# Kernel optimization log

Hardware: AMD Instinct MI355X
Metric: run time of the kernel (lower is better)

## Reference

```python
import jax, jax.numpy as jnp
import numpy as np

TOP_K = 512  # int(node_num * K) = int(2048 * 0.25)
NEG = -1.0e12
SLOPE = 0.01  # nn.LeakyReLU default negative_slope


def setup_inputs() -> dict:
    key = jax.random.key(0)
    k1, k2, k3, k4 = jax.random.split(key, 4)
    B, N, in_c, out_c, gs = 8, 2048, 128, 128, 128
    x = jax.random.normal(k1, (B, N, in_c), dtype=jnp.float32)
    W = jax.random.normal(k2, (in_c, out_c), dtype=jnp.float32) * (1.0 / np.sqrt(in_c))
    a = jax.random.normal(k3, (2 * out_c, 1), dtype=jnp.float32) * (1.0 / np.sqrt(2 * out_c))
    GL = jax.random.normal(k4, (N, gs), dtype=jnp.float32) * (1.0 / np.sqrt(gs))
    return {"x": x, "W": W, "a": a, "GL": GL}


def reference(x, W, a, GL):
    B, N, _ = x.shape
    out_c = W.shape[1]
    # learned adjacency: softmax(relu(GL GL^T)) + I  -> [N, N]
    adj = jax.nn.softmax(jax.nn.relu(GL @ GL.T), axis=-1) + jnp.eye(N, dtype=GL.dtype)
    h = x @ W  # [B, N, out_c]
    # e[b,i,j] = LeakyReLU( [h_i ; h_j] . a ) = LeakyReLU( h_i.a1 + h_j.a2 )
    # (avoids materializing the [B, N*N, 2*out_c] concat of the original)
    a1, a2 = a[:out_c, 0], a[out_c:, 0]
    e = jax.nn.leaky_relu((h @ a1)[:, :, None] + (h @ a2)[:, None, :], SLOPE)  # [B,N,N]
    att = jnp.where(adj[None] > 0, e, NEG)
    # top-k along dim=1 (rows, per column j): transpose so that axis is last
    att_t = jnp.swapaxes(att, 1, 2)  # [B, Nj, Ni]
    _, idx = jax.lax.top_k(att_t, TOP_K)  # idx: [B, Nj, TOP_K]
    b_ix = jnp.arange(B)[:, None, None]
    j_ix = jnp.arange(N)[None, :, None]
    mask_t = jnp.zeros_like(att_t).at[b_ix, j_ix, idx].set(1.0)
    mask = jnp.swapaxes(mask_t, 1, 2)  # [B, Ni, Nj]
    att = jax.nn.softmax(att * mask, axis=2)
    h_prime = jax.nn.relu(att @ h)  # [B, N, out_c]
    return jnp.swapaxes(h_prime, -2, -1)  # [B, out_c, N]
```

## Files before the change

### kernel.cpp

```cpp
#include <hip/hip_runtime.h>
#include <math.h>


#define B_ 8
#define N_ 2048
#define C_ 128
#define TOPK_ 512
#define NCH_ 32
#define CL_ 64
#define NP1_ 2052
#define SORTB_ (2 * B_)

#define H_OFF    ((size_t)0)
#define P_OFF    (H_OFF + (size_t)B_*N_*C_)
#define Q_OFF    (P_OFF + (size_t)B_*N_)
#define QS_OFF   (Q_OFF + (size_t)B_*N_)
#define US_OFF   (QS_OFF + (size_t)B_*N_)
#define VS_OFF   (US_OFF + (size_t)B_*N_)
#define SRT_OFF  (VS_OFF + (size_t)B_*N_)
#define SUS_OFF  (SRT_OFF + (size_t)B_*N_)
#define PVS_OFF  (SUS_OFF + (size_t)B_*NP1_)
#define SUL_OFF  (PVS_OFF + (size_t)B_*NP1_)
#define PVL_OFF  (SUL_OFF + (size_t)B_*N_*128)
#define TOTU_OFF (PVL_OFF + (size_t)B_*N_*128)
#define TOTV_OFF (TOTU_OFF + (size_t)B_*NCH_*128)
#define MPART_OFF (TOTV_OFF + (size_t)B_*NCH_*128)
#define PTHR_OFF (MPART_OFF + (size_t)B_*32*C_)
#define ITHR_OFF (PTHR_OFF + (size_t)B_)

__device__ __forceinline__ unsigned enc_f(float f) {
  unsigned b = __float_as_uint(f);
  return b ^ ((b >> 31) ? 0xFFFFFFFFu : 0x80000000u);
}
__device__ __forceinline__ float dec_f(unsigned e) {
  unsigned b = (e & 0x80000000u) ? (e ^ 0x80000000u) : ~e;
  return __uint_as_float(b);
}
__device__ __forceinline__ unsigned long long sxor64(unsigned long long v, int m) {
  int lo = __shfl_xor((int)(unsigned)(v & 0xffffffffULL), m, 64);
  int hi = __shfl_xor((int)(unsigned)(v >> 32), m, 64);
  return (((unsigned long long)(unsigned)hi) << 32) | (unsigned)lo;
}
__device__ __forceinline__ void cswap2(unsigned long long& a, unsigned long long& b, bool up) {
  bool sw = up ? (a > b) : (b > a);
  if (sw) { unsigned long long tm = a; a = b; b = tm; }
}

__global__ __launch_bounds__(256) void k_pq(const float* __restrict__ x,
                                            const float* __restrict__ W,
                                            const float* __restrict__ a,
                                            float* __restrict__ p,
                                            float* __restrict__ q) {
  __shared__ float al[256];
  __shared__ float wa1[128], wa2[128];
  const int t = threadIdx.x;
  const int r0 = blockIdx.x * 64;
  al[t] = a[t];
  __syncthreads();
  if (t < 128) {
    const float* Wr = W + (size_t)t * 128;
    float s1 = 0.f, s2 = 0.f;
#pragma unroll
    for (int j = 0; j < 128; j += 4) {
      float4 wv = *(const float4*)(Wr + j);
      s1 = fmaf(wv.x, al[j + 0], s1);
      s1 = fmaf(wv.y, al[j + 1], s1);
      s1 = fmaf(wv.z, al[j + 2], s1);
      s1 = fmaf(wv.w, al[j + 3], s1);
      s2 = fmaf(wv.x, al[128 + j + 0], s2);
      s2 = fmaf(wv.y, al[128 + j + 1], s2);
      s2 = fmaf(wv.z, al[128 + j + 2], s2);
      s2 = fmaf(wv.w, al[128 + j + 3], s2);
    }
    wa1[t] = s1; wa2[t] = s2;
  }
  __syncthreads();
  const int row = t >> 2, part = t & 3;
  const float* xr = x + (size_t)(r0 + row) * 128 + part * 32;
  const float* w1 = wa1 + part * 32;
  const float* w2 = wa2 + part * 32;
  float sp = 0.f, sq = 0.f;
#pragma unroll
  for (int i = 0; i < 8; ++i) {
    float4 xv = *(const float4*)(xr + 4 * i);
    float4 w1v = *(const float4*)(w1 + 4 * i);
    float4 w2v = *(const float4*)(w2 + 4 * i);
    sp = fmaf(xv.x, w1v.x, sp); sp = fmaf(xv.y, w1v.y, sp);
    sp = fmaf(xv.z, w1v.z, sp); sp = fmaf(xv.w, w1v.w, sp);
    sq = fmaf(xv.x, w2v.x, sq); sq = fmaf(xv.y, w2v.y, sq);
    sq = fmaf(xv.z, w2v.z, sq); sq = fmaf(xv.w, w2v.w, sq);
  }
  sp += __shfl_xor(sp, 1, 64); sp += __shfl_xor(sp, 2, 64);
  sq += __shfl_xor(sq, 1, 64); sq += __shfl_xor(sq, 2, 64);
  if (part == 0) { p[r0 + row] = sp; q[r0 + row] = sq; }
}

__global__ __launch_bounds__(512, 4) void k_fuse(
    const float* __restrict__ x, const float* __restrict__ W,
    float* __restrict__ h, float* __restrict__ mpart,
    const float* __restrict__ q, const float* __restrict__ p,
    float* __restrict__ q_s, float* __restrict__ u_s, float* __restrict__ v_s,
    int* __restrict__ srt, float* __restrict__ SUS, float* __restrict__ PVS,
    float* __restrict__ pthr, int* __restrict__ ithr) {
  union __align__(16) SMem {
    struct { float Wl[64 * 128]; float xl[64 * 68]; } g;
    struct { unsigned long long sh[N_]; float2 sa[512]; float2 sb[512]; } s;
  };
  __shared__ SMem sm;
  const int blk = blockIdx.x, t = threadIdx.x;

  if (blk < SORTB_) {
    const bool isP = blk >= B_;
    const int b = isP ? blk - B_ : blk;
    const float* src = isP ? p : q;
    float4 f4 = *(const float4*)(src + b * N_ + 4 * t);
    unsigned k0 = enc_f(f4.x), k1 = enc_f(f4.y), k2 = enc_f(f4.z), k3 = enc_f(f4.w);
    if (isP) { k0 = ~k0; k1 = ~k1; k2 = ~k2; k3 = ~k3; }
    unsigned long long r[4];
    r[0] = ((unsigned long long)k0 << 32) | (unsigned)(4 * t);
    r[1] = ((unsigned long long)k1 << 32) | (unsigned)(4 * t + 1);
    r[2] = ((unsigned long long)k2 << 32) | (unsigned)(4 * t + 2);
    r[3] = ((unsigned long long)k3 << 32) | (unsigned)(4 * t + 3);

    cswap2(r[0], r[1], true);
    cswap2(r[2], r[3], false);
    {
      const bool up4 = (t & 1) == 0;
      cswap2(r[0], r[2], up4); cswap2(r[1], r[3], up4);
      cswap2(r[0], r[1], up4); cswap2(r[2], r[3], up4);
    }
    for (int k = 8; k <= N_; k <<= 1) {
      const bool up = ((4 * t) & k) == 0;
      int j = k >> 1;
      for (; j >= 256; j >>= 1) {
        *(ulonglong2*)(sm.s.sh + 4 * t) = make_ulonglong2(r[0], r[1]);
        *(ulonglong2*)(sm.s.sh + 4 * t + 2) = make_ulonglong2(r[2], r[3]);
        __syncthreads();
        int pt = t ^ (j >> 2);
        ulonglong2 pa = *(const ulonglong2*)(sm.s.sh + 4 * pt);
        ulonglong2 pb = *(const ulonglong2*)(sm.s.sh + 4 * pt + 2);
        bool lower = (t & (j >> 2)) == 0;
        bool kmin = (up == lower);
        r[0] = kmin ? (r[0] < pa.x ? r[0] : pa.x) : (r[0] > pa.x ? r[0] : pa.x);
        r[1] = kmin ? (r[1] < pa.y ? r[1] : pa.y) : (r[1] > pa.y ? r[1] : pa.y);
        r[2] = kmin ? (r[2] < pb.x ? r[2] : pb.x) : (r[2] > pb.x ? r[2] : pb.x);
        r[3] = kmin ? (r[3] < pb.y ? r[3] : pb.y) : (r[3] > pb.y ? r[3] : pb.y);
        __syncthreads();
      }
      for (; j >= 4; j >>= 1) {
        int ld = j >> 2;
        unsigned long long p0 = sxor64(r[0], ld), p1 = sxor64(r[1], ld);
        unsigned long long p2 = sxor64(r[2], ld), p3 = sxor64(r[3], ld);
        bool lower = (t & ld) == 0;
        bool kmin = (up == lower);
        r[0] = kmin ? (r[0] < p0 ? r[0] : p0) : (r[0] > p0 ? r[0] : p0);
        r[1] = kmin ? (r[1] < p1 ? r[1] : p1) : (r[1] > p1 ? r[1] : p1);
        r[2] = kmin ? (r[2] < p2 ? r[2] : p2) : (r[2] > p2 ? r[2] : p2);
        r[3] = kmin ? (r[3] < p3 ? r[3] : p3) : (r[3] > p3 ? r[3] : p3);
      }
      cswap2(r[0], r[2], up); cswap2(r[1], r[3], up);
      cswap2(r[0], r[1], up); cswap2(r[2], r[3], up);
    }

    if (isP) {
      if (t == 127) {
        unsigned key = (unsigned)(r[3] >> 32);
        pthr[b] = dec_f(~key);
        ithr[b] = (int)(unsigned)(r[3] & 0xffffffffULL);
      }
      return;
    }
    float v[4], u[4], w[4]; int id[4];
#pragma unroll
    for (int s = 0; s < 4; ++s) {
      v[s] = dec_f((unsigned)(r[s] >> 32));
      id[s] = (int)(unsigned)(r[s] & 0xffffffffULL);
      u[s] = __expf(v[s]);
      w[s] = __expf(0.01f * v[s]);
    }
    *(float4*)(q_s + b * N_ + 4 * t) = make_float4(v[0], v[1], v[2], v[3]);
    *(float4*)(u_s + b * N_ + 4 * t) = make_float4(u[0], u[1], u[2], u[3]);
    *(float4*)(v_s + b * N_ + 4 * t) = make_float4(w[0], w[1], w[2], w[3]);
    *(int4*)(srt + b * N_ + 4 * t) = make_int4(id[0], id[1], id[2], id[3]);
    float pu = u[0] + u[1] + u[2] + u[3];
    float pw = w[0] + w[1] + w[2] + w[3];
    sm.s.sa[511 - t].x = pu;
    sm.s.sa[t].y = pw;
    __syncthreads();
    float2* cur = sm.s.sa; float2* nxt = sm.s.sb;
    for (int off = 1; off < 512; off <<= 1) {
      float2 vv = cur[t];
      if (t >= off) { float2 o = cur[t - off]; vv.x += o.x; vv.y += o.y; }
      nxt[t] = vv;
      __syncthreads();
      float2* tmp = cur; cur = nxt; nxt = tmp;
    }
    float PSt = cur[511 - t].x;
    float PPt = cur[t].y;
    float su0 = PSt;
    float su1 = su0 - u[0];
    float su2 = su1 - u[1];
    float su3 = su2 - u[2];
    *(float4*)(SUS + (size_t)b * NP1_ + 4 * t) = make_float4(su0, su1, su2, su3);
    float pv3 = PPt - w[3];
    float pv2 = pv3 - w[2];
    float pv1 = pv2 - w[1];
    float pv0 = pv1 - w[0];
    *(float4*)(PVS + (size_t)b * NP1_ + 4 * t) = make_float4(pv0, pv1, pv2, pv3);
    if (t == 511) {
      SUS[(size_t)b * NP1_ + N_] = 0.f;
      PVS[(size_t)b * NP1_ + N_] = PPt;
    }
    return;
  }

  float* Wl = sm.g.Wl;
  float* xl = sm.g.xl;
  const int g = blk - SORTB_;
  const int r0 = g * 64;
  const int cg = t & 15, rp = (t >> 4) & 15;
  const bool act = t < 256;
  float acc[4][8];
#pragma unroll
  for (int r = 0; r < 4; ++r)
#pragma unroll
    for (int j = 0; j < 8; ++j) acc[r][j] = 0.f;

  for (int kc = 0; kc < 2; ++kc) {
    __syncthreads();
    const float4* W4 = (const float4*)(W + (size_t)kc * 64 * 128);
    float4* Wl4 = (float4*)Wl;
#pragma unroll
    for (int i = 0; i < 4; ++i) Wl4[t + 512 * i] = W4[t + 512 * i];
#pragma unroll
    for (int i = 0; i < 2; ++i) {
      int idx = t + 512 * i;
      int row = idx >> 4, c4i = idx & 15;
      float4 v = *(const float4*)(x + (size_t)(r0 + row) * 128 + kc * 64 + c4i * 4);
      ((float4*)xl)[row * 17 + c4i] = v;
    }
    __syncthreads();
    if (act) {
      for (int k = 0; k < 64; ++k) {
        const float4* Wr = (const float4*)(Wl + k * 128);
        float4 w0 = Wr[cg];
        float4 w1 = Wr[cg + 16];
#pragma unroll
        for (int r = 0; r < 4; ++r) {
          float xv = xl[(4 * rp + r) * 68 + k];
          acc[r][0] = fmaf(xv, w0.x, acc[r][0]);
          acc[r][1] = fmaf(xv, w0.y, acc[r][1]);
          acc[r][2] = fmaf(xv, w0.z, acc[r][2]);
          acc[r][3] = fmaf(xv, w0.w, acc[r][3]);
          acc[r][4] = fmaf(xv, w1.x, acc[r][4]);
          acc[r][5] = fmaf(xv, w1.y, acc[r][5]);
          acc[r][6] = fmaf(xv, w1.z, acc[r][6]);
          acc[r][7] = fmaf(xv, w1.w, acc[r][7]);
        }
      }
    }
  }
  const int c0 = 4 * cg, c1 = 4 * cg + 64;
  size_t hb = (size_t)r0 * 128;
  __syncthreads();
  float* scratch = xl;
  if (act) {
#pragma unroll
    for (int r = 0; r < 4; ++r) {
      int row = 4 * rp + r;
      *(float4*)(h + hb + (size_t)row * 128 + c0) =
          make_float4(acc[r][0], acc[r][1], acc[r][2], acc[r][3]);
      *(float4*)(h + hb + (size_t)row * 128 + c1) =
          make_float4(acc[r][4], acc[r][5], acc[r][6], acc[r][7]);
    }
#pragma unroll
    for (int j = 0; j < 4; ++j) {
      scratch[rp * 128 + c0 + j] = acc[0][j] + acc[1][j] + acc[2][j] + acc[3][j];
      scratch[rp * 128 + c1 + j] = acc[0][4 + j] + acc[1][4 + j] + acc[2][4 + j] + acc[3][4 + j];
    }
  }
  __syncthreads();
  if (t < 128) {
    float s = 0.f;
#pragma unroll
    for (int rr = 0; rr < 16; ++rr) s += scratch[rr * 128 + t];
    mpart[(size_t)g * 128 + t] = s;
  }
}

__global__ __launch_bounds__(256) void k_scanA(const float* __restrict__ h,
                                               const float* __restrict__ u_s,
                                               const float* __restrict__ v_s,
                                               const int* __restrict__ srt,
                                               float* __restrict__ SUl,
                                               float* __restrict__ PVl,
                                               float* __restrict__ totU,
                                               float* __restrict__ totV) {
  __shared__ float hl[CL_][128];
  __shared__ float ul[CL_], vl[CL_];
  __shared__ int sl[CL_];
  const int b = blockIdx.x >> 5, ch = blockIdx.x & 31;
  const int t = threadIdx.x;
  const int base = b * N_ + ch * CL_;
  if (t < CL_) { ul[t] = u_s[base + t]; vl[t] = v_s[base + t]; sl[t] = srt[base + t]; }
  __syncthreads();
  {
    const int c4 = t & 31, rr = t >> 5;
#pragma unroll
    for (int i = 0; i < 8; ++i) {
      int tt = rr + 8 * i;
      float4 v = *(const float4*)(h + ((size_t)b * N_ + sl[tt]) * 128 + 4 * c4);
      *(float4*)(&hl[tt][4 * c4]) = v;
    }
  }
  __syncthreads();
  if (t < 128) {
    const int c = t;
    float run = 0.f;
    for (int tt = CL_ - 1; tt >= 0; --tt) {
      run = fmaf(ul[tt], hl[tt][c], run);
      SUl[((size_t)(base + tt)) * 128 + c] = run;
    }
    totU[(size_t)(b * NCH_ + ch) * 128 + c] = run;
  } else {
    const int c = t - 128;
    float run2 = 0.f;
    for (int tt = 0; tt < CL_; ++tt) {
      PVl[((size_t)(base + tt)) * 128 + c] = run2;
      run2 = fmaf(vl[tt], hl[tt][c], run2);
    }
    totV[(size_t)(b * NCH_ + ch) * 128 + c] = run2;
  }
}

__global__ __launch_bounds__(256) void k_out(const float* __restrict__ p,
                                             const float* __restrict__ q_s,
                                             const float* __restrict__ pthr,
                                             const int* __restrict__ ithr,
                                             const float* __restrict__ SUS,
                                             const float* __restrict__ PVS,
                                             const float* __restrict__ SUl,
                                             const float* __restrict__ PVl,
                                             const float* __restrict__ totU,
                                             const float* __restrict__ totV,
                                             const float* __restrict__ mpart,
                                             float* __restrict__ out) {
  __shared__ float qs_l[N_];
  __shared__ float res[64 * 129];
  __shared__ float CSUs[(NCH_ + 1) * 128];
  __shared__ float CPVs[(NCH_ + 1) * 128];
  __shared__ float mr[128];
  __shared__ float A_s[64], B_s[64], invD[64];
  __shared__ int lo_s[64], keep_s[64];
  const int b = blockIdx.x >> 5, tile = blockIdx.x & 31;
  const int t = threadIdx.x;
  const int i0 = tile * 64;
  for (int i = t; i < N_; i += 256) qs_l[i] = q_s[b * N_ + i];
  if (t < 128) {
    float ms = 0.f;
#pragma unroll
    for (int j = 0; j < 32; ++j) ms += mpart[(size_t)(b * 32 + j) * 128 + t];
    mr[t] = fmaxf(ms * (1.0f / (float)N_), 0.f);
    float s = 0.f;
    CSUs[NCH_ * 128 + t] = 0.f;
    for (int cc = NCH_ - 1; cc >= 0; --cc) {
      s += totU[(size_t)(b * NCH_ + cc) * 128 + t];
      CSUs[cc * 128 + t] = s;
    }
  } else {
    const int c2 = t - 128;
    float s2 = 0.f;
    for (int cc = 0; cc < NCH_; ++cc) {
      CPVs[cc * 128 + c2] = s2;
      s2 += totV[(size_t)(b * NCH_ + cc) * 128 + c2];
    }
    CPVs[NCH_ * 128 + c2] = s2;
  }
  __syncthreads();
  if (t < 64) {
    float pv = p[b * N_ + i0 + t];
    float thrv = pthr[b]; int thri = ithr[b];
    bool keep = (pv > thrv) || (pv == thrv && (i0 + t) <= thri);
    keep_s[t] = keep ? 1 : 0;
    float thr = -pv;
    int lo = 0, hi = N_;
    while (lo < hi) { int mid = (lo + hi) >> 1; if (qs_l[mid] < thr) lo = mid + 1; else hi = mid; }
    lo_s[t] = lo;
    float A = __expf(pv), Bv = __expf(0.01f * pv);
    A_s[t] = A; B_s[t] = Bv;
    float sus = SUS[(size_t)b * NP1_ + lo];
    float pvs = PVS[(size_t)b * NP1_ + lo];
    invD[t] = 1.0f / fmaf(A, sus, Bv * pvs);
  }
  __syncthreads();
  const int half = t >> 7, c = t & 127;
#pragma unroll 4
  for (int ii2 = 0; ii2 < 64; ii2 += 2) {
    int ii = ii2 + half;
    float outv;
    if (keep_s[ii]) {
      int lo = lo_s[ii];
      float A = A_s[ii], Bv = B_s[ii];
      float suc, pvc;
      if (lo < N_) {
        int chn = lo >> 6;
        size_t ro = ((size_t)(b * N_ + lo)) * 128;
        suc = SUl[ro + c] + CSUs[(chn + 1) * 128 + c];
        pvc = PVl[ro + c] + CPVs[chn * 128 + c];
      } else {
        suc = 0.f;
        pvc = CPVs[NCH_ * 128 + c];
      }
      outv = fmaxf(fmaf(A, suc, Bv * pvc) * invD[ii], 0.f);
    } else {
      outv = mr[c];
    }
    res[ii * 129 + c] = outv;
  }
  __syncthreads();
#pragma unroll
  for (int pass = 0; pass < 8; ++pass) {
    int cc = (t >> 4) + pass * 16;
    int ii4 = (t & 15) * 4;
    float4 v;
    v.x = res[(ii4 + 0) * 129 + cc];
    v.y = res[(ii4 + 1) * 129 + cc];
    v.z = res[(ii4 + 2) * 129 + cc];
    v.w = res[(ii4 + 3) * 129 + cc];
    *(float4*)(out + ((size_t)(b * C_ + cc)) * N_ + i0 + ii4) = v;
  }
}

extern "C" void kernel_launch(void* const* d_in, const int* in_sizes, int n_in,
                              void* d_out, int out_size, void* d_ws, size_t ws_size,
                              hipStream_t stream) {
  (void)in_sizes; (void)n_in; (void)out_size; (void)ws_size;
  const float* x = (const float*)d_in[0];
  const float* W = (const float*)d_in[1];
  const float* a = (const float*)d_in[2];
  float* out = (float*)d_out;
  float* ws = (float*)d_ws;

  float* h    = ws + H_OFF;
  float* p    = ws + P_OFF;
  float* q    = ws + Q_OFF;
  float* q_s  = ws + QS_OFF;
  float* u_s  = ws + US_OFF;
  float* v_s  = ws + VS_OFF;
  int*   srt  = (int*)(ws + SRT_OFF);
  float* SUS  = ws + SUS_OFF;
  float* PVS  = ws + PVS_OFF;
  float* SUl  = ws + SUL_OFF;
  float* PVl  = ws + PVL_OFF;
  float* totU = ws + TOTU_OFF;
  float* totV = ws + TOTV_OFF;
  float* mpart = ws + MPART_OFF;
  float* pthr = ws + PTHR_OFF;
  int*   ithr = (int*)(ws + ITHR_OFF);

  k_pq<<<dim3((B_ * N_) / 64), dim3(256), 0, stream>>>(x, W, a, p, q);
  k_fuse<<<dim3(SORTB_ + (B_ * N_) / 64), dim3(512), 0, stream>>>(
      x, W, h, mpart, q, p, q_s, u_s, v_s, srt, SUS, PVS, pthr, ithr);
  k_scanA<<<dim3(B_ * NCH_), dim3(256), 0, stream>>>(h, u_s, v_s, srt, SUl, PVl, totU, totV);
  k_out<<<dim3(B_ * 32), dim3(256), 0, stream>>>(p, q_s, pthr, ithr, SUS, PVS, SUl, PVl, totU, totV, mpart, out);
}
```

Measured before the change: 106.3 us.

## Replace per-batch bitonic sorts with parallel rank-counting across 256 blocks

Drops the 16 single-block bitonic sorts of q and p, which ran with many block-wide barriers. In their place, 256 blocks compute each element's rank, its lower-bound position and its top-k membership by brute-force counting over the row in shared memory, then scatter into sorted order. The prefix sums of the exponentials move into extra blocks of the scan kernel, and the binary search in k_out becomes a load of a packed word. This trades O(N^2) comparisons for much more parallelism and fewer serialized sync steps on the critical path.

```diff
diff --git a/kernel.cpp b/kernel.cpp
--- a/kernel.cpp
+++ b/kernel.cpp
@@ -9,13 +9,13 @@
 #define NCH_ 32
 #define CL_ 64
 #define NP1_ 2052
-#define SORTB_ (2 * B_)
+#define RANKB_ 256
 
 #define H_OFF    ((size_t)0)
 #define P_OFF    (H_OFF + (size_t)B_*N_*C_)
 #define Q_OFF    (P_OFF + (size_t)B_*N_)
-#define QS_OFF   (Q_OFF + (size_t)B_*N_)
-#define US_OFF   (QS_OFF + (size_t)B_*N_)
+#define LOK_OFF  (Q_OFF + (size_t)B_*N_)
+#define US_OFF   (LOK_OFF + (size_t)B_*N_)
 #define VS_OFF   (US_OFF + (size_t)B_*N_)
 #define SRT_OFF  (VS_OFF + (size_t)B_*N_)
 #define SUS_OFF  (SRT_OFF + (size_t)B_*N_)
@@ -25,26 +25,6 @@
 #define TOTU_OFF (PVL_OFF + (size_t)B_*N_*128)
 #define TOTV_OFF (TOTU_OFF + (size_t)B_*NCH_*128)
 #define MPART_OFF (TOTV_OFF + (size_t)B_*NCH_*128)
-#define PTHR_OFF (MPART_OFF + (size_t)B_*32*C_)
-#define ITHR_OFF (PTHR_OFF + (size_t)B_)
-
-__device__ __forceinline__ unsigned enc_f(float f) {
-  unsigned b = __float_as_uint(f);
-  return b ^ ((b >> 31) ? 0xFFFFFFFFu : 0x80000000u);
-}
-__device__ __forceinline__ float dec_f(unsigned e) {
-  unsigned b = (e & 0x80000000u) ? (e ^ 0x80000000u) : ~e;
-  return __uint_as_float(b);
-}
-__device__ __forceinline__ unsigned long long sxor64(unsigned long long v, int m) {
-  int lo = __shfl_xor((int)(unsigned)(v & 0xffffffffULL), m, 64);
-  int hi = __shfl_xor((int)(unsigned)(v >> 32), m, 64);
-  return (((unsigned long long)(unsigned)hi) << 32) | (unsigned)lo;
-}
-__device__ __forceinline__ void cswap2(unsigned long long& a, unsigned long long& b, bool up) {
-  bool sw = up ? (a > b) : (b > a);
-  if (sw) { unsigned long long tm = a; a = b; b = tm; }
-}
 
 __global__ __launch_bounds__(256) void k_pq(const float* __restrict__ x,
                                             const float* __restrict__ W,
@@ -99,124 +79,58 @@
     const float* __restrict__ x, const float* __restrict__ W,
     float* __restrict__ h, float* __restrict__ mpart,
     const float* __restrict__ q, const float* __restrict__ p,
-    float* __restrict__ q_s, float* __restrict__ u_s, float* __restrict__ v_s,
-    int* __restrict__ srt, float* __restrict__ SUS, float* __restrict__ PVS,
-    float* __restrict__ pthr, int* __restrict__ ithr) {
+    float* __restrict__ u_s, float* __restrict__ v_s,
+    int* __restrict__ srt, int* __restrict__ lok) {
   union __align__(16) SMem {
     struct { float Wl[64 * 128]; float xl[64 * 68]; } g;
-    struct { unsigned long long sh[N_]; float2 sa[512]; float2 sb[512]; } s;
+    struct { float ql[N_]; float pl[N_]; } r;
   };
   __shared__ SMem sm;
   const int blk = blockIdx.x, t = threadIdx.x;
 
-  if (blk < SORTB_) {
-    const bool isP = blk >= B_;
-    const int b = isP ? blk - B_ : blk;
-    const float* src = isP ? p : q;
-    float4 f4 = *(const float4*)(src + b * N_ + 4 * t);
-    unsigned k0 = enc_f(f4.x), k1 = enc_f(f4.y), k2 = enc_f(f4.z), k3 = enc_f(f4.w);
-    if (isP) { k0 = ~k0; k1 = ~k1; k2 = ~k2; k3 = ~k3; }
-    unsigned long long r[4];
-    r[0] = ((unsigned long long)k0 << 32) | (unsigned)(4 * t);
-    r[1] = ((unsigned long long)k1 << 32) | (unsigned)(4 * t + 1);
-    r[2] = ((unsigned long long)k2 << 32) | (unsigned)(4 * t + 2);
-    r[3] = ((unsigned long long)k3 << 32) | (unsigned)(4 * t + 3);
-
-    cswap2(r[0], r[1], true);
-    cswap2(r[2], r[3], false);
-    {
-      const bool up4 = (t & 1) == 0;
-      cswap2(r[0], r[2], up4); cswap2(r[1], r[3], up4);
-      cswap2(r[0], r[1], up4); cswap2(r[2], r[3], up4);
-    }
-    for (int k = 8; k <= N_; k <<= 1) {
-      const bool up = ((4 * t) & k) == 0;
-      int j = k >> 1;
-      for (; j >= 256; j >>= 1) {
-        *(ulonglong2*)(sm.s.sh + 4 * t) = make_ulonglong2(r[0], r[1]);
-        *(ulonglong2*)(sm.s.sh + 4 * t + 2) = make_ulonglong2(r[2], r[3]);
-        __syncthreads();
-        int pt = t ^ (j >> 2);
-        ulonglong2 pa = *(const ulonglong2*)(sm.s.sh + 4 * pt);
-        ulonglong2 pb = *(const ulonglong2*)(sm.s.sh + 4 * pt + 2);
-        bool lower = (t & (j >> 2)) == 0;
-        bool kmin = (up == lower);
-        r[0] = kmin ? (r[0] < pa.x ? r[0] : pa.x) : (r[0] > pa.x ? r[0] : pa.x);
-        r[1] = kmin ? (r[1] < pa.y ? r[1] : pa.y) : (r[1] > pa.y ? r[1] : pa.y);
-        r[2] = kmin ? (r[2] < pb.x ? r[2] : pb.x) : (r[2] > pb.x ? r[2] : pb.x);
-        r[3] = kmin ? (r[3] < pb.y ? r[3] : pb.y) : (r[3] > pb.y ? r[3] : pb.y);
-        __syncthreads();
-      }
-      for (; j >= 4; j >>= 1) {
-        int ld = j >> 2;
-        unsigned long long p0 = sxor64(r[0], ld), p1 = sxor64(r[1], ld);
-        unsigned long long p2 = sxor64(r[2], ld), p3 = sxor64(r[3], ld);
-        bool lower = (t & ld) == 0;
-        bool kmin = (up == lower);
-        r[0] = kmin ? (r[0] < p0 ? r[0] : p0) : (r[0] > p0 ? r[0] : p0);
-        r[1] = kmin ? (r[1] < p1 ? r[1] : p1) : (r[1] > p1 ? r[1] : p1);
-        r[2] = kmin ? (r[2] < p2 ? r[2] : p2) : (r[2] > p2 ? r[2] : p2);
-        r[3] = kmin ? (r[3] < p3 ? r[3] : p3) : (r[3] > p3 ? r[3] : p3);
-      }
-      cswap2(r[0], r[2], up); cswap2(r[1], r[3], up);
-      cswap2(r[0], r[1], up); cswap2(r[2], r[3], up);
-    }
-
-    if (isP) {
-      if (t == 127) {
-        unsigned key = (unsigned)(r[3] >> 32);
-        pthr[b] = dec_f(~key);
-        ithr[b] = (int)(unsigned)(r[3] & 0xffffffffULL);
-      }
-      return;
-    }
-    float v[4], u[4], w[4]; int id[4];
-#pragma unroll
-    for (int s = 0; s < 4; ++s) {
-      v[s] = dec_f((unsigned)(r[s] >> 32));
-      id[s] = (int)(unsigned)(r[s] & 0xffffffffULL);
-      u[s] = __expf(v[s]);
-      w[s] = __expf(0.01f * v[s]);
-    }
-    *(float4*)(q_s + b * N_ + 4 * t) = make_float4(v[0], v[1], v[2], v[3]);
-    *(float4*)(u_s + b * N_ + 4 * t) = make_float4(u[0], u[1], u[2], u[3]);
-    *(float4*)(v_s + b * N_ + 4 * t) = make_float4(w[0], w[1], w[2], w[3]);
-    *(int4*)(srt + b * N_ + 4 * t) = make_int4(id[0], id[1], id[2], id[3]);
-    float pu = u[0] + u[1] + u[2] + u[3];
-    float pw = w[0] + w[1] + w[2] + w[3];
-    sm.s.sa[511 - t].x = pu;
-    sm.s.sa[t].y = pw;
+  if (blk < RANKB_) {
+    const int b = blk >> 5, tile = blk & 31;
+    const int i0 = tile * 64;
+    ((float4*)sm.r.ql)[t] = ((const float4*)(q + (size_t)b * N_))[t];
+    ((float4*)sm.r.pl)[t] = ((const float4*)(p + (size_t)b * N_))[t];
     __syncthreads();
-    float2* cur = sm.s.sa; float2* nxt = sm.s.sb;
-    for (int off = 1; off < 512; off <<= 1) {
-      float2 vv = cur[t];
-      if (t >= off) { float2 o = cur[t - off]; vv.x += o.x; vv.y += o.y; }
-      nxt[t] = vv;
-      __syncthreads();
-      float2* tmp = cur; cur = nxt; nxt = tmp;
-    }
-    float PSt = cur[511 - t].x;
-    float PPt = cur[t].y;
-    float su0 = PSt;
-    float su1 = su0 - u[0];
-    float su2 = su1 - u[1];
-    float su3 = su2 - u[2];
-    *(float4*)(SUS + (size_t)b * NP1_ + 4 * t) = make_float4(su0, su1, su2, su3);
-    float pv3 = PPt - w[3];
-    float pv2 = pv3 - w[2];
-    float pv1 = pv2 - w[1];
-    float pv0 = pv1 - w[0];
-    *(float4*)(PVS + (size_t)b * NP1_ + 4 * t) = make_float4(pv0, pv1, pv2, pv3);
-    if (t == 511) {
-      SUS[(size_t)b * NP1_ + N_] = 0.f;
-      PVS[(size_t)b * NP1_ + N_] = PPt;
+    const int row = t >> 3, s = t & 7;
+    const int i = i0 + row;
+    const float qi = sm.r.ql[i], pi = sm.r.pl[i];
+    const float negpi = -pi;
+    int qr = 0, lo = 0, pr = 0;
+    for (int g = s; g < 512; g += 8) {
+      float4 qj = ((const float4*)sm.r.ql)[g];
+      float4 pj = ((const float4*)sm.r.pl)[g];
+      const int j0 = 4 * g;
+      qr += (qj.x < qi || (qj.x == qi && (j0 + 0) < i)) ? 1 : 0;
+      qr += (qj.y < qi || (qj.y == qi && (j0 + 1) < i)) ? 1 : 0;
+      qr += (qj.z < qi || (qj.z == qi && (j0 + 2) < i)) ? 1 : 0;
+      qr += (qj.w < qi || (qj.w == qi && (j0 + 3) < i)) ? 1 : 0;
+      lo += (qj.x < negpi) ? 1 : 0;
+      lo += (qj.y < negpi) ? 1 : 0;
+      lo += (qj.z < negpi) ? 1 : 0;
+      lo += (qj.w < negpi) ? 1 : 0;
+      pr += (pj.x > pi || (pj.x == pi && (j0 + 0) < i)) ? 1 : 0;
+      pr += (pj.y > pi || (pj.y == pi && (j0 + 1) < i)) ? 1 : 0;
+      pr += (pj.z > pi || (pj.z == pi && (j0 + 2) < i)) ? 1 : 0;
+      pr += (pj.w > pi || (pj.w == pi && (j0 + 3) < i)) ? 1 : 0;
+    }
+    qr += __shfl_xor(qr, 1, 64); qr += __shfl_xor(qr, 2, 64); qr += __shfl_xor(qr, 4, 64);
+    lo += __shfl_xor(lo, 1, 64); lo += __shfl_xor(lo, 2, 64); lo += __shfl_xor(lo, 4, 64);
+    pr += __shfl_xor(pr, 1, 64); pr += __shfl_xor(pr, 2, 64); pr += __shfl_xor(pr, 4, 64);
+    if (s == 0) {
+      u_s[(size_t)b * N_ + qr] = __expf(qi);
+      v_s[(size_t)b * N_ + qr] = __expf(0.01f * qi);
+      srt[(size_t)b * N_ + qr] = i;
+      lok[(size_t)b * N_ + i] = lo | ((pr < TOPK_) ? 0x10000 : 0);
     }
     return;
   }
 
   float* Wl = sm.g.Wl;
   float* xl = sm.g.xl;
-  const int g = blk - SORTB_;
+  const int g = blk - RANKB_;
   const int r0 = g * 64;
   const int cg = t & 15, rp = (t >> 4) & 15;
   const bool act = t < 256;
@@ -288,19 +202,61 @@
   }
 }
 
-__global__ __launch_bounds__(256) void k_scanA(const float* __restrict__ h,
-                                               const float* __restrict__ u_s,
-                                               const float* __restrict__ v_s,
-                                               const int* __restrict__ srt,
-                                               float* __restrict__ SUl,
-                                               float* __restrict__ PVl,
-                                               float* __restrict__ totU,
-                                               float* __restrict__ totV) {
+__global__ __launch_bounds__(256) void k_scan(const float* __restrict__ h,
+                                              const float* __restrict__ u_s,
+                                              const float* __restrict__ v_s,
+                                              const int* __restrict__ srt,
+                                              float* __restrict__ SUl,
+                                              float* __restrict__ PVl,
+                                              float* __restrict__ totU,
+                                              float* __restrict__ totV,
+                                              float* __restrict__ SUS,
+                                              float* __restrict__ PVS) {
   __shared__ float hl[CL_][128];
   __shared__ float ul[CL_], vl[CL_];
   __shared__ int sl[CL_];
+  __shared__ float2 sa[256], sb[256];
+  const int t = threadIdx.x;
+  if (blockIdx.x >= 256) {
+    const int b = blockIdx.x - 256;
+    float4 ua = ((const float4*)(u_s + (size_t)b * N_))[2 * t];
+    float4 ub = ((const float4*)(u_s + (size_t)b * N_))[2 * t + 1];
+    float4 wa = ((const float4*)(v_s + (size_t)b * N_))[2 * t];
+    float4 wb = ((const float4*)(v_s + (size_t)b * N_))[2 * t + 1];
+    float su = ua.x + ua.y + ua.z + ua.w + ub.x + ub.y + ub.z + ub.w;
+    float sw = wa.x + wa.y + wa.z + wa.w + wb.x + wb.y + wb.z + wb.w;
+    sa[t] = make_float2(su, sw);
+    __syncthreads();
+    float2* cur = sa; float2* nxt = sb;
+    for (int off = 1; off < 256; off <<= 1) {
+      float2 vv = cur[t];
+      if (t >= off) { float2 o = cur[t - off]; vv.x += o.x; vv.y += o.y; }
+      nxt[t] = vv;
+      __syncthreads();
+      float2* tmp = cur; cur = nxt; nxt = tmp;
+    }
+    float2 incl = cur[t];
+    float2 tot = cur[255];
+    float exclU = incl.x - su, exclW = incl.y - sw;
+    float s0 = tot.x - exclU;
+    float s1 = s0 - ua.x, s2 = s1 - ua.y, s3 = s2 - ua.z;
+    float s4 = s3 - ua.w, s5 = s4 - ub.x, s6 = s5 - ub.y, s7 = s6 - ub.z;
+    float p0 = exclW;
+    float p1 = p0 + wa.x, p2 = p1 + wa.y, p3 = p2 + wa.z;
+    float p4 = p3 + wa.w, p5 = p4 + wb.x, p6 = p5 + wb.y, p7 = p6 + wb.z;
+    float* Sb = SUS + (size_t)b * NP1_ + 8 * t;
+    float* Pb = PVS + (size_t)b * NP1_ + 8 * t;
+    *(float4*)(Sb) = make_float4(s0, s1, s2, s3);
+    *(float4*)(Sb + 4) = make_float4(s4, s5, s6, s7);
+    *(float4*)(Pb) = make_float4(p0, p1, p2, p3);
+    *(float4*)(Pb + 4) = make_float4(p4, p5, p6, p7);
+    if (t == 255) {
+      SUS[(size_t)b * NP1_ + N_] = 0.f;
+      PVS[(size_t)b * NP1_ + N_] = tot.y;
+    }
+    return;
+  }
   const int b = blockIdx.x >> 5, ch = blockIdx.x & 31;
-  const int t = threadIdx.x;
   const int base = b * N_ + ch * CL_;
   if (t < CL_) { ul[t] = u_s[base + t]; vl[t] = v_s[base + t]; sl[t] = srt[base + t]; }
   __syncthreads();
@@ -334,9 +290,7 @@
 }
 
 __global__ __launch_bounds__(256) void k_out(const float* __restrict__ p,
-                                             const float* __restrict__ q_s,
-                                             const float* __restrict__ pthr,
-                                             const int* __restrict__ ithr,
+                                             const int* __restrict__ lok,
                                              const float* __restrict__ SUS,
                                              const float* __restrict__ PVS,
                                              const float* __restrict__ SUl,
@@ -345,7 +299,6 @@
                                              const float* __restrict__ totV,
                                              const float* __restrict__ mpart,
                                              float* __restrict__ out) {
-  __shared__ float qs_l[N_];
   __shared__ float res[64 * 129];
   __shared__ float CSUs[(NCH_ + 1) * 128];
   __shared__ float CPVs[(NCH_ + 1) * 128];
@@ -355,7 +308,6 @@
   const int b = blockIdx.x >> 5, tile = blockIdx.x & 31;
   const int t = threadIdx.x;
   const int i0 = tile * 64;
-  for (int i = t; i < N_; i += 256) qs_l[i] = q_s[b * N_ + i];
   if (t < 128) {
     float ms = 0.f;
 #pragma unroll
@@ -379,12 +331,9 @@
   __syncthreads();
   if (t < 64) {
     float pv = p[b * N_ + i0 + t];
-    float thrv = pthr[b]; int thri = ithr[b];
-    bool keep = (pv > thrv) || (pv == thrv && (i0 + t) <= thri);
-    keep_s[t] = keep ? 1 : 0;
-    float thr = -pv;
-    int lo = 0, hi = N_;
-    while (lo < hi) { int mid = (lo + hi) >> 1; if (qs_l[mid] < thr) lo = mid + 1; else hi = mid; }
+    int lk = lok[(size_t)b * N_ + i0 + t];
+    keep_s[t] = (lk >> 16) & 1;
+    int lo = lk & 0xFFFF;
     lo_s[t] = lo;
     float A = __expf(pv), Bv = __expf(0.01f * pv);
     A_s[t] = A; B_s[t] = Bv;
@@ -444,7 +393,7 @@
   float* h    = ws + H_OFF;
   float* p    = ws + P_OFF;
   float* q    = ws + Q_OFF;
-  float* q_s  = ws + QS_OFF;
+  int*   lok  = (int*)(ws + LOK_OFF);
   float* u_s  = ws + US_OFF;
   float* v_s  = ws + VS_OFF;
   int*   srt  = (int*)(ws + SRT_OFF);
@@ -455,12 +404,10 @@
   float* totU = ws + TOTU_OFF;
   float* totV = ws + TOTV_OFF;
   float* mpart = ws + MPART_OFF;
-  float* pthr = ws + PTHR_OFF;
-  int*   ithr = (int*)(ws + ITHR_OFF);
 
   k_pq<<<dim3((B_ * N_) / 64), dim3(256), 0, stream>>>(x, W, a, p, q);
-  k_fuse<<<dim3(SORTB_ + (B_ * N_) / 64), dim3(512), 0, stream>>>(
-      x, W, h, mpart, q, p, q_s, u_s, v_s, srt, SUS, PVS, pthr, ithr);
-  k_scanA<<<dim3(B_ * NCH_), dim3(256), 0, stream>>>(h, u_s, v_s, srt, SUl, PVl, totU, totV);
-  k_out<<<dim3(B_ * 32), dim3(256), 0, stream>>>(p, q_s, pthr, ithr, SUS, PVS, SUl, PVl, totU, totV, mpart, out);
+  k_fuse<<<dim3(RANKB_ + (B_ * N_) / 64), dim3(512), 0, stream>>>(
+      x, W, h, mpart, q, p, u_s, v_s, srt, lok);
+  k_scan<<<dim3(256 + B_), dim3(256), 0, stream>>>(h, u_s, v_s, srt, SUl, PVl, totU, totV, SUS, PVS);
+  k_out<<<dim3(B_ * 32), dim3(256), 0, stream>>>(p, lok, SUS, PVS, SUl, PVl, totU, totV, mpart, out);
 }
```

Result: no change. 104.3 us (median of 2 runs) (-1.9%).
